# Kernel tuning notes

Measured on AMD Instinct MI355X. Metric: run time of the kernel, lower is better.

## Reference

```python
import jax, jax.numpy as jnp
import numpy as np

EMBED_DIM = 1536
NUM_HEADS = 12
HEAD_DIM = EMBED_DIM // NUM_HEADS  # 128
SEQ = 2048
EPS = 1e-5


def rms_norm(x, w):
    # x: (..., HEAD_DIM)
    var = jnp.mean(jnp.square(x), axis=-1, keepdims=True)
    return x * jax.lax.rsqrt(var + EPS) * w


def apply_rotary(x, cos, sin):
    # x: (b, s, h, d); cos/sin: (s, d/2) -> broadcast (1, s, 1, d/2)
    d2 = cos.shape[-1]
    c = cos[None, :, None, :]
    s_ = sin[None, :, None, :]
    x1, x2 = x[..., :d2], x[..., d2:]
    return jnp.concatenate([x1 * c - x2 * s_, x2 * c + x1 * s_], axis=-1)


def setup_inputs() -> dict:
    key = jax.random.key(0)
    ks = jax.random.split(key, 10)
    x = jax.random.normal(ks[0], (SEQ, 1, EMBED_DIM), dtype=jnp.float32)
    cu_seqlens = jnp.array([0, SEQ // 2, SEQ], dtype=jnp.int32)
    # rotary tables for positions 0..SEQ-1, rotary dim = HEAD_DIM
    inv_freq = 1.0 / (10000.0 ** (jnp.arange(0, HEAD_DIM, 2, dtype=jnp.float32) / HEAD_DIM))
    pos = jnp.arange(SEQ, dtype=jnp.float32)
    freqs = pos[:, None] * inv_freq[None, :]  # (s, d/2)
    rotary_pos_emb_cos = jnp.cos(freqs)
    rotary_pos_emb_sin = jnp.sin(freqs)
    scale = 0.02
    w_qkv = jax.random.normal(ks[1], (EMBED_DIM, 3 * EMBED_DIM), dtype=jnp.float32) * scale
    b_qkv = jnp.zeros((3 * EMBED_DIM,), dtype=jnp.float32)
    q_norm_w = jnp.ones((HEAD_DIM,), dtype=jnp.float32)
    k_norm_w = jnp.ones((HEAD_DIM,), dtype=jnp.float32)
    w_proj = jax.random.normal(ks[2], (EMBED_DIM, EMBED_DIM), dtype=jnp.float32) * scale
    b_proj = jnp.zeros((EMBED_DIM,), dtype=jnp.float32)
    return {
        'x': x, 'cu_seqlens': cu_seqlens,
        'rotary_pos_emb_cos': rotary_pos_emb_cos, 'rotary_pos_emb_sin': rotary_pos_emb_sin,
        'w_qkv': w_qkv, 'b_qkv': b_qkv, 'q_norm_w': q_norm_w, 'k_norm_w': k_norm_w,
        'w_proj': w_proj, 'b_proj': b_proj,
    }


def reference(x, cu_seqlens, rotary_pos_emb_cos, rotary_pos_emb_sin,
              w_qkv, b_qkv, q_norm_w, k_norm_w, w_proj, b_proj):
    s, b, e = x.shape
    h, d = NUM_HEADS, HEAD_DIM
    qkv = jnp.einsum('sbe,ef->sbf', x, w_qkv) + b_qkv  # (s, b, 3e)
    q, k, v = jnp.split(qkv, 3, axis=2)
    q = q.reshape(s, b, h, d)
    k = k.reshape(s, b, h, d)
    v = v.reshape(s, b, h, d)
    # per-head RMSNorm on q/k
    q = rms_norm(q, q_norm_w)
    k = rms_norm(k, k_norm_w)
    # (s, b, h, d) -> (b, s, h, d)
    q = jnp.transpose(q, (1, 0, 2, 3))
    k = jnp.transpose(k, (1, 0, 2, 3))
    v = jnp.transpose(v, (1, 0, 2, 3))
    q = apply_rotary(q, rotary_pos_emb_cos, rotary_pos_emb_sin)
    k = apply_rotary(k, rotary_pos_emb_cos, rotary_pos_emb_sin)
    # varlen (block-diagonal, non-causal) attention via segment mask
    pos = jnp.arange(s)
    seg = jnp.searchsorted(cu_seqlens[1:], pos, side='right')  # (s,)
    mask = seg[:, None] == seg[None, :]  # (s, s)
    scale = d ** -0.5
    scores = jnp.einsum('bqhd,bkhd->bhqk', q, k) * scale  # (b, h, s, s)
    scores = jnp.where(mask[None, None, :, :], scores, jnp.finfo(scores.dtype).min)
    attn = jax.nn.softmax(scores, axis=-1)
    ctx = jnp.einsum('bhqk,bkhd->bqhd', attn, v)  # (b, s, h, d)
    # (b, s, h, d) -> (s, b, h*d)
    ctx = jnp.transpose(ctx, (1, 0, 2, 3)).reshape(s, b, h * d)
    out = jnp.einsum('sbe,ef->sbf', ctx, w_proj) + b_proj
    return out
```

## Files before the change

### kernel.cpp

```cpp
#include <hip/hip_runtime.h>
#include <hip/hip_bf16.h>
#include <stdint.h>

#define S_LEN 2048
#define EMB   1536
#define NH    12
#define HD    128
#define N3    4608
#define RMS_EPS 1e-5f
#define ATTN_SCALE 0.08838834764831845f
#define SPLIT 2
#define LOG2E 1.44269504088896f
#define DEFER_THR 11.5416f

typedef short short8_t __attribute__((ext_vector_type(8)));
typedef float f32x4    __attribute__((ext_vector_type(4)));

typedef __attribute__((address_space(1))) const void g1_void;
typedef __attribute__((address_space(3))) void l3_void;

__device__ __forceinline__ void gload_lds16(const void* g, void* l) {
  __builtin_amdgcn_global_load_lds((g1_void*)g, (l3_void*)l, 16, 0, 0);
}

__device__ __forceinline__ short f2bf(float f) {
  union { float f; unsigned u; } v; v.f = f;
  unsigned r = (v.u + 0x7FFFu + ((v.u >> 16) & 1u)) >> 16;
  return (short)(r & 0xFFFFu);
}
__device__ __forceinline__ float bf2f(short s) {
  union { unsigned u; float f; } v; v.u = ((unsigned)(unsigned short)s) << 16;
  return v.f;
}

__global__ __launch_bounds__(256) void k_cvt_bf16(const float* __restrict__ in,
                                                  short* __restrict__ out, int n) {
  int i = (blockIdx.x * 256 + threadIdx.x) * 4;
  if (i + 3 < n) {
    float4 v = *(const float4*)(in + i);
    short4 o;
    o.x = f2bf(v.x); o.y = f2bf(v.y); o.z = f2bf(v.z); o.w = f2bf(v.w);
    *(short4*)(out + i) = o;
  }
}

__global__ __launch_bounds__(256) void k_transpose_cvt(const float* __restrict__ W,
                                                       short* __restrict__ Wt,
                                                       int K, int N) {
  __shared__ float t[32][33];
  int n0 = blockIdx.x * 32, k0 = blockIdx.y * 32;
  int tx = threadIdx.x, ty = threadIdx.y;
#pragma unroll
  for (int r = 0; r < 4; ++r) {
    int k = ty + r * 8;
    t[k][tx] = W[(size_t)(k0 + k) * N + n0 + tx];
  }
  __syncthreads();
#pragma unroll
  for (int r = 0; r < 4; ++r) {
    int j = ty + r * 8;
    Wt[(size_t)(n0 + j) * K + k0 + tx] = f2bf(t[tx][j]);
  }
}

template<bool OBF>
__global__ __launch_bounds__(256, 4) void k_gemm_v3(const short* __restrict__ A,
                                                    const short* __restrict__ Bt,
                                                    const float* __restrict__ bias,
                                                    void* __restrict__ Cv,
                                                    int M, int N, int K) {
  __shared__ short lds[2][128 * 64];
  const int tid = threadIdx.x;
  const int lane = tid & 63, wid = tid >> 6;
  const int wr = (wid >> 1) * 64, wc = (wid & 1) * 64;
  const int bn = blockIdx.x * 128, bm = blockIdx.y * 128;
  const int lr = lane & 15, lg = lane >> 4;
  const int swz = (lr & 7) << 4;

  const int srow = lane >> 3;
  const int skc  = ((lane & 7) ^ srow) * 8;

  f32x4 acc[4][4] = {};
  const int nk = K >> 6;

  for (int t = 0; t < nk; ++t) {
    const int kt = t << 6;
    __syncthreads();
#pragma unroll
    for (int it = 0; it < 4; ++it) {
      int seg = wid * 4 + it;
      int row = seg * 8 + srow;
      gload_lds16(A  + (size_t)(bm + row) * K + kt + skc, &lds[0][seg * 512]);
      gload_lds16(Bt + (size_t)(bn + row) * K + kt + skc, &lds[1][seg * 512]);
    }
    __syncthreads();
    const char* baseA = (const char*)&lds[0][0];
    const char* baseB = (const char*)&lds[1][0];
#pragma unroll
    for (int kk = 0; kk < 2; ++kk) {
      short8_t af[4], bfr[4];
#pragma unroll
      for (int m = 0; m < 4; ++m) {
        int row = wr + m * 16 + lr;
        af[m] = *(const short8_t*)(baseA + ((row * 128 + kk * 64 + lg * 16) ^ swz));
      }
#pragma unroll
      for (int n = 0; n < 4; ++n) {
        int row = wc + n * 16 + lr;
        bfr[n] = *(const short8_t*)(baseB + ((row * 128 + kk * 64 + lg * 16) ^ swz));
      }
#pragma unroll
      for (int m = 0; m < 4; ++m)
#pragma unroll
        for (int n = 0; n < 4; ++n)
          acc[m][n] = __builtin_amdgcn_mfma_f32_16x16x32_bf16(af[m], bfr[n], acc[m][n], 0, 0, 0);
    }
  }

#pragma unroll
  for (int m = 0; m < 4; ++m)
#pragma unroll
    for (int n = 0; n < 4; ++n) {
      int col = bn + wc + n * 16 + lr;
      float bv = bias[col];
#pragma unroll
      for (int r = 0; r < 4; ++r) {
        int row = bm + wr + m * 16 + lg * 4 + r;
        float v = acc[m][n][r] + bv;
        if (OBF) ((short*)Cv)[(size_t)row * N + col] = f2bf(v);
        else     ((float*)Cv)[(size_t)row * N + col] = v;
      }
    }
}

__global__ __launch_bounds__(256) void k_post(const short* __restrict__ qkv,
                                              const float* __restrict__ cosv,
                                              const float* __restrict__ sinv,
                                              const float* __restrict__ qw,
                                              const float* __restrict__ kw,
                                              short* __restrict__ qb,
                                              short* __restrict__ kb,
                                              short* __restrict__ vt) {
  __shared__ short ldsv[64 * 130];
  const int h = blockIdx.x, s0 = blockIdx.y * 64;
  const int t = threadIdx.x;
  const int r = t >> 2, j = t & 3;
  const int s = s0 + r;
  const size_t rowbase = (size_t)s * N3 + h * HD;
  const float SC2 = ATTN_SCALE * LOG2E;

  {
    const short* vp = qkv + rowbase + 2 * EMB + j * 32;
#pragma unroll
    for (int i4 = 0; i4 < 4; ++i4)
      *(short8_t*)&ldsv[r * 130 + j * 32 + i4 * 8] = *(const short8_t*)(vp + i4 * 8);
  }

#pragma unroll
  for (int qk = 0; qk < 2; ++qk) {
    const short* p = qkv + rowbase + qk * EMB + j * 32;
    const float* w = qk ? kw : qw;
    float v[32];
#pragma unroll
    for (int i4 = 0; i4 < 4; ++i4) {
      short8_t x = *(const short8_t*)(p + i4 * 8);
#pragma unroll
      for (int e = 0; e < 8; ++e) v[i4 * 8 + e] = bf2f(x[e]);
    }
    float ss = 0.f;
#pragma unroll
    for (int i = 0; i < 32; ++i) ss += v[i] * v[i];
    ss += __shfl_xor(ss, 1);
    ss += __shfl_xor(ss, 2);
    float rsq = rsqrtf(ss * (1.0f / HD) + RMS_EPS);
    if (qk == 0) rsq *= SC2;
#pragma unroll
    for (int i = 0; i < 32; ++i) v[i] = v[i] * rsq * w[j * 32 + i];
    const float* cp = cosv + (size_t)s * 64 + (j & 1) * 32;
    const float* sp = sinv + (size_t)s * 64 + (j & 1) * 32;
    short out[32];
#pragma unroll
    for (int i = 0; i < 32; ++i) {
      float part = __shfl_xor(v[i], 2);
      float c = cp[i], sn = sp[i];
      float o = (j < 2) ? (v[i] * c - part * sn) : (v[i] * c + part * sn);
      out[i] = f2bf(o);
    }
    short* dst = (qk ? kb : qb) + ((size_t)h * S_LEN + s) * HD + j * 32;
#pragma unroll
    for (int i4 = 0; i4 < 4; ++i4) {
      short8_t o8;
#pragma unroll
      for (int e = 0; e < 8; ++e) o8[e] = out[i4 * 8 + e];
      *(short8_t*)(dst + i4 * 8) = o8;
    }
  }

  __syncthreads();
  const int sl = t & 63, wv = t >> 6;
#pragma unroll
  for (int it = 0; it < 32; ++it) {
    int d = it * 4 + wv;
    vt[((size_t)h * HD + d) * S_LEN + s0 + sl] = ldsv[sl * 130 + d];
  }
}

__global__ __launch_bounds__(512, 2) void k_attn(const short* __restrict__ qb,
                                                 const short* __restrict__ kb,
                                                 const short* __restrict__ vt,
                                                 const int* __restrict__ cu, int nseg,
                                                 short* __restrict__ Opart,
                                                 float* __restrict__ mlpart) {
  __shared__ short ldsK[2][8192];
  __shared__ short ldsV[2][128 * 64];
  __shared__ short ldsP[8 * 16 * 64];

  const int wg = blockIdx.x;
  const int member = wg / 48;
  const int c = wg % 48;
  const int p = c & 1;
  const int h = c >> 2;
  const int qt = ((c >> 1) & 1) * 8 + member;

  const int q0 = qt * 128;
  const int tid = threadIdx.x, l = tid & 63, w = tid >> 6;
  const int lr = l & 15, lg = l >> 4;

  const short* kb_h = kb + (size_t)h * S_LEN * HD;
  const short* vt_h = vt + (size_t)h * HD * S_LEN;

  const int qrow_sm = q0 + w * 16 + lr;
  int segq = 0;
  for (int i = 1; i <= nseg; ++i) if (qrow_sm >= cu[i]) segq = i;
  const int rs_s = (segq == 0) ? 0 : cu[segq];
  const int re_s = (segq < nseg) ? cu[segq + 1] : S_LEN;
  float m = -INFINITY, lsum = 0.f;

  int seg0 = 0, seg1 = 0;
  for (int i = 1; i <= nseg; ++i) {
    if (q0 >= cu[i]) seg0 = i;
    if (q0 + 127 >= cu[i]) seg1 = i;
  }
  const int ks = (seg0 == 0) ? 0 : cu[seg0];
  const int ke = (seg1 < nseg) ? cu[seg1 + 1] : S_LEN;
  const int kt0 = (ks >> 6) << 6;
  const int nt = (ke - kt0 + 63) >> 6;
  const int tpb = (nt + SPLIT - 1) / SPLIT;
  const int tb0 = p * tpb;
  const int tb1 = (tb0 + tpb < nt) ? tb0 + tpb : nt;

  const int vseg_row = l >> 3;

  short8_t qf[4];
  {
    int srow = q0 + w * 16 + lr;
    const short* qp = qb + ((size_t)h * S_LEN + srow) * HD;
#pragma unroll
    for (int kk = 0; kk < 4; ++kk)
      qf[kk] = *(const short8_t*)(qp + kk * 32 + lg * 8);
  }

  f32x4 cacc[8] = {};

#define STAGE(kt_, buf_)                                                          \
  {                                                                               \
    const int kt__ = (kt_);                                                       \
    _Pragma("unroll")                                                             \
    for (int it = 0; it < 2; ++it) {                                              \
      int s = w * 2 + it;                                                         \
      int half = s >> 3;                                                          \
      int krow = (s & 7) * 8 + (l >> 3);                                          \
      int kc = half * 64 + (((l & 7) ^ (l >> 3)) * 8);                            \
      gload_lds16(kb_h + (size_t)(kt__ + krow) * HD + kc, &ldsK[buf_][s * 512]);  \
      int drow = s * 8 + vseg_row;                                                \
      int sv = ((l & 7) ^ (drow & 7)) * 8;                                        \
      gload_lds16(vt_h + (size_t)drow * S_LEN + kt__ + sv, &ldsV[buf_][s * 512]); \
    }                                                                             \
  }

  if (tb0 < tb1)     STAGE(kt0 + tb0 * 64, 0);
  if (tb0 + 1 < tb1) {
    STAGE(kt0 + (tb0 + 1) * 64, 1);
    asm volatile("s_waitcnt vmcnt(4)" ::: "memory");
  } else {
    asm volatile("s_waitcnt vmcnt(0)" ::: "memory");
  }
  __builtin_amdgcn_s_barrier();

  int cur = 0;
  for (int ti = tb0; ti < tb1; ++ti) {
    const int kt = kt0 + ti * 64;
    const char* bK = (const char*)&ldsK[cur][0];
    const char* bV = (const char*)&ldsV[cur][0];

    f32x4 sacc[4] = {};
    __builtin_amdgcn_s_setprio(1);
#pragma unroll
    for (int n = 0; n < 4; ++n) {
#pragma unroll
      for (int kk = 0; kk < 4; ++kk) {
        int row = n * 16 + lr;
        int byte = (kk >> 1) * 8192 + row * 128 + (kk & 1) * 64 + lg * 16;
        byte ^= (lr & 7) << 4;
        short8_t kf = *(const short8_t*)(bK + byte);
        sacc[n] = __builtin_amdgcn_mfma_f32_16x16x32_bf16(kf, qf[kk], sacc[n], 0, 0, 0);
      }
    }
    __builtin_amdgcn_s_setprio(0);

    if (!__all((kt >= rs_s) && (kt + 64 <= re_s))) {
#pragma unroll
      for (int n = 0; n < 4; ++n) {
        int kbase = kt + n * 16 + lg * 4;
#pragma unroll
        for (int r = 0; r < 4; ++r) {
          int key = kbase + r;
          sacc[n][r] = (key >= rs_s && key < re_s) ? sacc[n][r] : -1e30f;
        }
      }
    }

    float tm = sacc[0][0];
#pragma unroll
    for (int n = 0; n < 4; ++n)
#pragma unroll
      for (int r = 0; r < 4; ++r) tm = fmaxf(tm, sacc[n][r]);
    tm = fmaxf(tm, __shfl_xor(tm, 16));
    tm = fmaxf(tm, __shfl_xor(tm, 32));

    if (!__all(tm <= m + DEFER_THR)) {
      float mn = fmaxf(m, tm);
      float alpha = exp2f(m - mn);
      m = mn;
      lsum *= alpha;
      float a[4];
#pragma unroll
      for (int r = 0; r < 4; ++r) a[r] = __shfl(alpha, lg * 4 + r);
#pragma unroll
      for (int n = 0; n < 8; ++n)
#pragma unroll
        for (int r = 0; r < 4; ++r) cacc[n][r] *= a[r];
    }

    float ls = 0.f;
#pragma unroll
    for (int n = 0; n < 4; ++n) {
      short4 p4;
      float p0 = exp2f(sacc[n][0] - m);
      float p1 = exp2f(sacc[n][1] - m);
      float p2 = exp2f(sacc[n][2] - m);
      float p3 = exp2f(sacc[n][3] - m);
      ls += (p0 + p1) + (p2 + p3);
      p4.x = f2bf(p0); p4.y = f2bf(p1); p4.z = f2bf(p2); p4.w = f2bf(p3);
      int byte = lr * 128 + (n * 16 + lg * 4) * 2;
      byte ^= (lr & 7) << 4;
      *(short4*)((char*)ldsP + w * 2048 + byte) = p4;
    }
    ls += __shfl_xor(ls, 16);
    ls += __shfl_xor(ls, 32);
    lsum += ls;

    __builtin_amdgcn_s_setprio(1);
#pragma unroll
    for (int kk = 0; kk < 2; ++kk) {
      int byteP = lr * 128 + (kk * 32 + lg * 8) * 2;
      byteP ^= (lr & 7) << 4;
      short8_t pf = *(const short8_t*)((const char*)ldsP + w * 2048 + byteP);
#pragma unroll
      for (int n = 0; n < 8; ++n) {
        int d = n * 16 + lr;
        int byteV = d * 128 + (kk * 32 + lg * 8) * 2;
        byteV ^= (d & 7) << 4;
        short8_t vf = *(const short8_t*)(bV + byteV);
        cacc[n] = __builtin_amdgcn_mfma_f32_16x16x32_bf16(pf, vf, cacc[n], 0, 0, 0);
      }
    }
    __builtin_amdgcn_s_setprio(0);

    __builtin_amdgcn_s_barrier();
    if (ti + 2 < tb1) {
      STAGE(kt0 + (ti + 2) * 64, cur);
      asm volatile("s_waitcnt vmcnt(4)" ::: "memory");
    } else {
      asm volatile("s_waitcnt vmcnt(0)" ::: "memory");
    }
    __builtin_amdgcn_s_barrier();
    cur ^= 1;
  }
#undef STAGE

  const int b = (h * 16 + qt) * SPLIT + p;
#pragma unroll
  for (int r = 0; r < 4; ++r) {
    int qrow = w * 16 + lg * 4 + r;
#pragma unroll
    for (int n = 0; n < 8; ++n)
      Opart[(size_t)b * 16384 + qrow * 128 + n * 16 + lr] = f2bf(cacc[n][r]);
  }
  if (lg == 0) {
    mlpart[(size_t)b * 256 + w * 16 + lr] = m;
    mlpart[(size_t)b * 256 + 128 + w * 16 + lr] = lsum;
  }
}

__global__ __launch_bounds__(512) void k_combine(const short* __restrict__ Opart,
                                                 const float* __restrict__ ml,
                                                 short* __restrict__ ctx) {
  const int h = blockIdx.x, qt = blockIdx.y, t = threadIdx.x;
  const int r = t >> 2, j = t & 3;
  const int b0 = (h * 16 + qt) * SPLIT;

  float mp[SPLIT], lp[SPLIT], wp[SPLIT];
  float M = -INFINITY;
#pragma unroll
  for (int p = 0; p < SPLIT; ++p) {
    mp[p] = ml[(size_t)(b0 + p) * 256 + r];
    lp[p] = ml[(size_t)(b0 + p) * 256 + 128 + r];
    M = fmaxf(M, mp[p]);
  }
  float L = 0.f;
#pragma unroll
  for (int p = 0; p < SPLIT; ++p) {
    wp[p] = exp2f(mp[p] - M);
    L += lp[p] * wp[p];
  }
  const float inv = 1.0f / L;

  float acc[32];
#pragma unroll
  for (int i = 0; i < 32; ++i) acc[i] = 0.f;
#pragma unroll
  for (int p = 0; p < SPLIT; ++p) {
    const short* src = Opart + (size_t)(b0 + p) * 16384 + r * 128 + j * 32;
#pragma unroll
    for (int i4 = 0; i4 < 4; ++i4) {
      short8_t v = *(const short8_t*)(src + i4 * 8);
#pragma unroll
      for (int e = 0; e < 8; ++e) acc[i4 * 8 + e] += wp[p] * bf2f(v[e]);
    }
  }

  short* dst = ctx + (size_t)(qt * 128 + r) * EMB + h * HD + j * 32;
#pragma unroll
  for (int i4 = 0; i4 < 4; ++i4) {
    short8_t o8;
#pragma unroll
    for (int e = 0; e < 8; ++e) o8[e] = f2bf(acc[i4 * 8 + e] * inv);
    *(short8_t*)(dst + i4 * 8) = o8;
  }
}

extern "C" void kernel_launch(void* const* d_in, const int* in_sizes, int n_in,
                              void* d_out, int out_size, void* d_ws, size_t ws_size,
                              hipStream_t stream) {
  const float* x      = (const float*)d_in[0];
  const int*   cu     = (const int*)d_in[1];
  const float* cosv   = (const float*)d_in[2];
  const float* sinv   = (const float*)d_in[3];
  const float* w_qkv  = (const float*)d_in[4];
  const float* b_qkv  = (const float*)d_in[5];
  const float* q_norm = (const float*)d_in[6];
  const float* k_norm = (const float*)d_in[7];
  const float* w_proj = (const float*)d_in[8];
  const float* b_proj = (const float*)d_in[9];
  const int nseg = in_sizes[1] - 1;

  char* ws = (char*)d_ws;
  short* xb     = (short*)(ws);
  short* wqkvT  = (short*)(ws + 6291456);
  short* wprojT = (short*)(ws + 20447232);
  short* qkv16  = (short*)(ws + 25165824);
  short* qb     = (short*)(ws + 44040192);
  short* kb     = (short*)(ws + 50331648);
  short* vt     = (short*)(ws + 56623104);
  short* ctxb   = (short*)(ws + 62914560);
  short* Opart  = qkv16;
  float* mlpart = (float*)ws;

  k_cvt_bf16<<<(S_LEN * EMB) / 1024, 256, 0, stream>>>(x, xb, S_LEN * EMB);
  k_transpose_cvt<<<dim3(N3 / 32, EMB / 32), dim3(32, 8), 0, stream>>>(w_qkv, wqkvT, EMB, N3);
  k_transpose_cvt<<<dim3(EMB / 32, EMB / 32), dim3(32, 8), 0, stream>>>(w_proj, wprojT, EMB, EMB);
  k_gemm_v3<true><<<dim3(N3 / 128, S_LEN / 128), 256, 0, stream>>>(xb, wqkvT, b_qkv, qkv16, S_LEN, N3, EMB);
  k_post<<<dim3(NH, S_LEN / 64), 256, 0, stream>>>(qkv16, cosv, sinv, q_norm, k_norm, qb, kb, vt);
  k_attn<<<dim3(NH * (S_LEN / 128) * SPLIT), 512, 0, stream>>>(qb, kb, vt, cu, nseg, Opart, mlpart);
  k_combine<<<dim3(NH, S_LEN / 128), 512, 0, stream>>>(Opart, mlpart, ctxb);
  k_gemm_v3<false><<<dim3(EMB / 128, S_LEN / 128), 256, 0, stream>>>(ctxb, wprojT, b_proj, (float*)d_out, S_LEN, EMB, EMB);
}
```

Measured before the change: 139.4 us.

## Double-buffer GEMM LDS tiles with async prefetch two stages ahead

Converts the bf16 GEMM from a single-buffered load-then-compute loop into a double-buffered pipeline: two K-tiles are prefetched into LDS via global_load_lds, and each iteration issues the load for tile t+2 into the buffer just consumed, using vmcnt waits and raw barriers. MFMA sections are wrapped in s_setprio to favour math waves. The aim is to hide global-memory latency behind MFMA work. LDS use doubles to 64KB per block and the occupancy hint drops from 4 to 2 blocks per CU.

```diff
diff --git a/kernel.cpp b/kernel.cpp
--- a/kernel.cpp
+++ b/kernel.cpp
@@ -64,12 +64,12 @@
 }
 
 template<bool OBF>
-__global__ __launch_bounds__(256, 4) void k_gemm_v3(const short* __restrict__ A,
+__global__ __launch_bounds__(256, 2) void k_gemm_v4(const short* __restrict__ A,
                                                     const short* __restrict__ Bt,
                                                     const float* __restrict__ bias,
                                                     void* __restrict__ Cv,
                                                     int M, int N, int K) {
-  __shared__ short lds[2][128 * 64];
+  __shared__ short lds[2][2][128 * 64];
   const int tid = threadIdx.x;
   const int lane = tid & 63, wid = tid >> 6;
   const int wr = (wid >> 1) * 64, wc = (wid & 1) * 64;
@@ -83,19 +83,32 @@
   f32x4 acc[4][4] = {};
   const int nk = K >> 6;
 
+#define GSTAGE(kt_, buf_)                                                          \
+  {                                                                                \
+    const int kt__ = (kt_);                                                        \
+    _Pragma("unroll")                                                              \
+    for (int it = 0; it < 4; ++it) {                                               \
+      int seg = wid * 4 + it;                                                      \
+      int row = seg * 8 + srow;                                                    \
+      gload_lds16(A  + (size_t)(bm + row) * K + kt__ + skc, &lds[buf_][0][seg * 512]); \
+      gload_lds16(Bt + (size_t)(bn + row) * K + kt__ + skc, &lds[buf_][1][seg * 512]); \
+    }                                                                              \
+  }
+
+  GSTAGE(0, 0);
+  if (nk > 1) {
+    GSTAGE(64, 1);
+    asm volatile("s_waitcnt vmcnt(8)" ::: "memory");
+  } else {
+    asm volatile("s_waitcnt vmcnt(0)" ::: "memory");
+  }
+  __builtin_amdgcn_s_barrier();
+
+  int cur = 0;
   for (int t = 0; t < nk; ++t) {
-    const int kt = t << 6;
-    __syncthreads();
-#pragma unroll
-    for (int it = 0; it < 4; ++it) {
-      int seg = wid * 4 + it;
-      int row = seg * 8 + srow;
-      gload_lds16(A  + (size_t)(bm + row) * K + kt + skc, &lds[0][seg * 512]);
-      gload_lds16(Bt + (size_t)(bn + row) * K + kt + skc, &lds[1][seg * 512]);
-    }
-    __syncthreads();
-    const char* baseA = (const char*)&lds[0][0];
-    const char* baseB = (const char*)&lds[1][0];
+    const char* baseA = (const char*)&lds[cur][0][0];
+    const char* baseB = (const char*)&lds[cur][1][0];
+    __builtin_amdgcn_s_setprio(1);
 #pragma unroll
     for (int kk = 0; kk < 2; ++kk) {
       short8_t af[4], bfr[4];
@@ -115,7 +128,19 @@
         for (int n = 0; n < 4; ++n)
           acc[m][n] = __builtin_amdgcn_mfma_f32_16x16x32_bf16(af[m], bfr[n], acc[m][n], 0, 0, 0);
     }
-  }
+    __builtin_amdgcn_s_setprio(0);
+
+    __builtin_amdgcn_s_barrier();
+    if (t + 2 < nk) {
+      GSTAGE((t + 2) << 6, cur);
+      asm volatile("s_waitcnt vmcnt(8)" ::: "memory");
+    } else {
+      asm volatile("s_waitcnt vmcnt(0)" ::: "memory");
+    }
+    __builtin_amdgcn_s_barrier();
+    cur ^= 1;
+  }
+#undef GSTAGE
 
 #pragma unroll
   for (int m = 0; m < 4; ++m)
@@ -480,9 +505,9 @@
   k_cvt_bf16<<<(S_LEN * EMB) / 1024, 256, 0, stream>>>(x, xb, S_LEN * EMB);
   k_transpose_cvt<<<dim3(N3 / 32, EMB / 32), dim3(32, 8), 0, stream>>>(w_qkv, wqkvT, EMB, N3);
   k_transpose_cvt<<<dim3(EMB / 32, EMB / 32), dim3(32, 8), 0, stream>>>(w_proj, wprojT, EMB, EMB);
-  k_gemm_v3<true><<<dim3(N3 / 128, S_LEN / 128), 256, 0, stream>>>(xb, wqkvT, b_qkv, qkv16, S_LEN, N3, EMB);
+  k_gemm_v4<true><<<dim3(N3 / 128, S_LEN / 128), 256, 0, stream>>>(xb, wqkvT, b_qkv, qkv16, S_LEN, N3, EMB);
   k_post<<<dim3(NH, S_LEN / 64), 256, 0, stream>>>(qkv16, cosv, sinv, q_norm, k_norm, qb, kb, vt);
   k_attn<<<dim3(NH * (S_LEN / 128) * SPLIT), 512, 0, stream>>>(qb, kb, vt, cu, nseg, Opart, mlpart);
   k_combine<<<dim3(NH, S_LEN / 128), 512, 0, stream>>>(Opart, mlpart, ctxb);
-  k_gemm_v3<false><<<dim3(EMB / 128, S_LEN / 128), 256, 0, stream>>>(ctxb, wprojT, b_proj, (float*)d_out, S_LEN, EMB, EMB);
-}
+  k_gemm_v4<false><<<dim3(EMB / 128, S_LEN / 128), 256, 0, stream>>>(ctxb, wprojT, b_proj, (float*)d_out, S_LEN, EMB, EMB);
+}
```

New measurement: 132.0 us. 1.06x faster.
